# Optimization experiments

Hardware: AMD Instinct MI355X
Metric: run time of the kernel (lower is better)

The kernel has to match this reference:

```python
import jax, jax.numpy as jnp
import numpy as np
import math

B, S, N_UNITS, D_K = 8, 2048, 1024, 512


def setup_inputs() -> dict:
    key = jax.random.key(0)
    ks = jax.random.split(key, 8)
    scale = 1.0 / math.sqrt(N_UNITS)
    query = jax.random.normal(ks[0], (B, S, N_UNITS), dtype=jnp.float32)
    k_in = jax.random.normal(ks[1], (B, S, N_UNITS), dtype=jnp.float32)
    v_in = jax.random.normal(ks[2], (B, S, N_UNITS), dtype=jnp.float32)
    # custom multiplicative mask: causal lower-triangular, broadcast over batch
    mask = jnp.broadcast_to(jnp.tril(jnp.ones((S, S), dtype=jnp.float32)), (B, S, S))
    Wq = jax.random.normal(ks[3], (N_UNITS, D_K), dtype=jnp.float32) * scale
    Wk = jax.random.normal(ks[4], (N_UNITS, D_K), dtype=jnp.float32) * scale
    Wv = jax.random.normal(ks[5], (N_UNITS, D_K), dtype=jnp.float32) * scale
    bq = jnp.zeros((D_K,), dtype=jnp.float32)
    bk = jnp.zeros((D_K,), dtype=jnp.float32)
    bv = jnp.zeros((D_K,), dtype=jnp.float32)
    return {"query": query, "key": k_in, "value": v_in, "mask": mask,
            "Wq": Wq, "bq": bq, "Wk": Wk, "bk": bk, "Wv": Wv, "bv": bv}


def reference(query, key, value, mask, Wq, bq, Wk, bk, Wv, bv):
    d_k = Wq.shape[-1]
    Q = jnp.einsum('bsn,nd->bsd', query, Wq) + bq  # [B,S,Dk]
    K = jnp.einsum('bsn,nd->bsd', key, Wk) + bk
    V = jnp.einsum('bsn,nd->bsd', value, Wv) + bv
    # scores [B,S,S]
    x_hat = jnp.einsum('bqd,bkd->bqk', Q, K) / jnp.sqrt(jnp.float32(d_k))
    # custom multiplicative mask: x*mask - 1e9*(1-mask)
    x_hat_masked = x_hat * mask - 1e9 * (1.0 - mask)
    attn = jax.nn.softmax(x_hat_masked, axis=-1)
    # dropout = 0.0 (eval mode) -> identity
    out = jnp.einsum('bqk,bkd->bqd', attn, V)
    return out
```

## Files before the change

### kernel.cpp

```cpp
#include <hip/hip_runtime.h>

typedef __bf16 bf16_t;
typedef __attribute__((ext_vector_type(4))) __bf16 bf16x4;
typedef __attribute__((ext_vector_type(8))) __bf16 bf16x8;
typedef __attribute__((ext_vector_type(4))) float f32x4;

#define B_    8
#define S_    2048
#define NU    1024
#define DK    512
#define MROWS (B_ * S_)
#define PBATCH (128 * 128 * 136)

#define WAITVM(N) asm volatile("s_waitcnt vmcnt(" #N ")" ::: "memory")
#define WAITLG    asm volatile("s_waitcnt lgkmcnt(0)" ::: "memory")
#define BAR       asm volatile("s_barrier" ::: "memory")

__device__ __forceinline__ f32x4 mfma16(bf16x8 a, bf16x8 b, f32x4 c) {
  return __builtin_amdgcn_mfma_f32_16x16x32_bf16(a, b, c, 0, 0, 0);
}

__device__ __forceinline__ void async_load16(const void* g, void* l) {
  __builtin_amdgcn_global_load_lds(
      (const __attribute__((address_space(1))) unsigned int*)g,
      (__attribute__((address_space(3))) unsigned int*)l, 16, 0, 0);
}

__device__ __forceinline__ bf16x8 cvt8(f32x4 x0, f32x4 x1) {
  bf16x8 r;
#pragma unroll
  for (int j = 0; j < 4; ++j) { r[j] = (bf16_t)x0[j]; r[j + 4] = (bf16_t)x1[j]; }
  return r;
}

__device__ __forceinline__ void stage_tile(const bf16_t* __restrict__ src,
                                           int rstride, bf16_t* dst, int k0,
                                           int tid) {
#pragma unroll
  for (int j = 0; j < 2; ++j) {
    const int g = j * 256 + tid;
    const int ln = g >> 3, c = g & 7;
    const int cs = c ^ (ln & 7);
    const int srow = 2 * ln + (cs >> 2);
    async_load16(src + (size_t)srow * rstride + k0 + (cs & 3) * 8, dst + g * 8);
  }
}

__device__ __forceinline__ void stage_tile64(const bf16_t* __restrict__ src,
                                             int rstride, bf16_t* dst, int k0,
                                             int tid) {
  const int ln = tid >> 3, c = tid & 7;
  const int cs = c ^ (ln & 7);
  const int srow = 2 * ln + (cs >> 2);
  async_load16(src + (size_t)srow * rstride + k0 + (cs & 3) * 8, dst + tid * 8);
}

__device__ __forceinline__ bf16x8 frag(const bf16_t* buf, int row, int q) {
  const int ln = row >> 1;
  const int cp = (((row & 1) << 2) | q) ^ (ln & 7);
  return *(const bf16x8*)(buf + ln * 64 + cp * 8);
}

__global__ __launch_bounds__(256) void transpose_w_kernel(
    const float* __restrict__ Wq, const float* __restrict__ Wk,
    const float* __restrict__ Wv, bf16_t* __restrict__ Wt) {
  const float* W = (blockIdx.z == 0) ? Wq : (blockIdx.z == 1) ? Wk : Wv;
  bf16_t* Wo = Wt + (size_t)blockIdx.z * DK * NU;
  __shared__ float tile[32][33];
  const int t = threadIdx.x;
  const int r = t >> 5, c = t & 31;
  const int kbase = blockIdx.y * 32, nbase = blockIdx.x * 32;
#pragma unroll
  for (int i = 0; i < 4; ++i)
    tile[r + i * 8][c] = W[(size_t)(kbase + r + i * 8) * DK + nbase + c];
  __syncthreads();
#pragma unroll
  for (int i = 0; i < 4; ++i)
    Wo[(size_t)(nbase + r + i * 8) * NU + kbase + c] = (bf16_t)tile[c][r + i * 8];
}

__global__ __launch_bounds__(256, 2) void xw3_gemm_kernel(
    const float* __restrict__ q_in, const float* __restrict__ k_in,
    const float* __restrict__ v_in, const bf16_t* __restrict__ Wt,
    const float* __restrict__ bq, const float* __restrict__ bk,
    const float* __restrict__ bv, bf16_t* __restrict__ Qo,
    bf16_t* __restrict__ Ko, bf16_t* __restrict__ Vt) {
  const int bx = blockIdx.x;
  const int z = bx >> 9;
  const int t = bx & 511;
  const int m0 = (t & 127) * 128;
  const int n0 = (t >> 7) * 128;
  const float* X = (z == 0) ? q_in : (z == 1) ? k_in : v_in;
  const float* bias = (z == 0) ? bq : (z == 1) ? bk : bv;

  const int tid = threadIdx.x;
  const int wave = tid >> 6, lane = tid & 63;
  const int l16 = lane & 15, quad = lane >> 4;
  const int wm = (wave >> 1) * 64, wn = (wave & 1) * 64;

  __shared__ __align__(16) unsigned char smem[65536];
  bf16_t* ldsA = (bf16_t*)smem;
  bf16_t* ldsB = (bf16_t*)(smem + 32768);

  const float* Ag = X + (size_t)m0 * NU;
  const bf16_t* Bg = Wt + (size_t)z * DK * NU + (size_t)n0 * NU;

  int g0 = 2 * tid, g1 = 2 * tid + 1;
  const int cs0 = (g0 & 7) ^ ((g0 >> 3) & 7);
  const int cs1 = (g1 & 7) ^ ((g1 >> 3) & 7);
  const int sr0 = 2 * (g0 >> 3) + (cs0 >> 2), c40 = cs0 & 3;
  const int sr1 = 2 * (g1 >> 3) + (cs1 >> 2), c41 = cs1 & 3;
  const float* ap0 = Ag + (size_t)sr0 * NU + c40 * 8;
  const float* ap1 = Ag + (size_t)sr1 * NU + c41 * 8;

#define XW_A_LOAD(S, K0)                                                      \
  f32x4 xl##S##0 = *(const f32x4*)(ap0 + (K0));                               \
  f32x4 xl##S##1 = *(const f32x4*)(ap0 + (K0) + 4);                           \
  f32x4 xl##S##2 = *(const f32x4*)(ap1 + (K0));                               \
  f32x4 xl##S##3 = *(const f32x4*)(ap1 + (K0) + 4);
#define XW_A_WRITE(S, BUFE)                                                   \
  *(bf16x8*)&ldsA[(BUFE) + g0 * 8] = cvt8(xl##S##0, xl##S##1);                \
  *(bf16x8*)&ldsA[(BUFE) + g1 * 8] = cvt8(xl##S##2, xl##S##3);

  f32x4 acc[4][4] = {};

  {
    XW_A_LOAD(0, 0)
    XW_A_LOAD(1, 32)
    XW_A_LOAD(2, 64)
    XW_A_LOAD(3, 96)
    stage_tile(Bg, NU, ldsB, 0, tid);
    stage_tile(Bg, NU, ldsB + 4096, 32, tid);
    stage_tile(Bg, NU, ldsB + 8192, 64, tid);
    stage_tile(Bg, NU, ldsB + 12288, 96, tid);
    XW_A_WRITE(0, 0)
    XW_A_WRITE(1, 4096)
    XW_A_WRITE(2, 8192)
    XW_A_WRITE(3, 12288)
    WAITVM(0);
    WAITLG;
    BAR;
  }

  const int NS = 32;
  for (int j = 0; j < NS / 2; ++j) {
    const int ks2 = 2 * j;
    const int base = (j & 1) * 8192;
    bf16x8 af[2][4], bfr[2][4];
#pragma unroll
    for (int s = 0; s < 2; ++s)
#pragma unroll
      for (int i = 0; i < 4; ++i) {
        af[s][i] = frag(ldsA + base + s * 4096, wm + i * 16 + l16, quad);
        bfr[s][i] = frag(ldsB + base + s * 4096, wn + i * 16 + l16, quad);
      }
    WAITLG;
    BAR;
    const bool more = (ks2 + 4) < NS;
    if (more) {
      const int k4 = (ks2 + 4) * 32;
      XW_A_LOAD(4, k4)
      XW_A_LOAD(5, k4 + 32)
      stage_tile(Bg, NU, ldsB + base, k4, tid);
      stage_tile(Bg, NU, ldsB + base + 4096, k4 + 32, tid);
      __builtin_amdgcn_s_setprio(1);
#pragma unroll
      for (int s = 0; s < 2; ++s)
#pragma unroll
        for (int i = 0; i < 4; ++i)
#pragma unroll
          for (int jj = 0; jj < 4; ++jj)
            acc[i][jj] = mfma16(af[s][i], bfr[s][jj], acc[i][jj]);
      __builtin_amdgcn_s_setprio(0);
      WAITVM(4);
      XW_A_WRITE(4, base)
      XW_A_WRITE(5, base + 4096)
    } else {
      __builtin_amdgcn_s_setprio(1);
#pragma unroll
      for (int s = 0; s < 2; ++s)
#pragma unroll
        for (int i = 0; i < 4; ++i)
#pragma unroll
          for (int jj = 0; jj < 4; ++jj)
            acc[i][jj] = mfma16(af[s][i], bfr[s][jj], acc[i][jj]);
      __builtin_amdgcn_s_setprio(0);
      WAITVM(0);
    }
    WAITLG;
    BAR;
  }

  if (z != 2) {
    bf16_t* Out = (z == 0) ? Qo : Ko;
#pragma unroll
    for (int j = 0; j < 4; ++j) {
      const int cn = n0 + wn + j * 16 + l16;
      const float bz = bias[cn];
#pragma unroll
      for (int i = 0; i < 4; ++i) {
        const int rm = m0 + wm + i * 16 + quad * 4;
#pragma unroll
        for (int r = 0; r < 4; ++r)
          Out[(size_t)(rm + r) * DK + cn] = (bf16_t)(acc[i][j][r] + bz);
      }
    }
  } else {
    bf16_t* Ts = (bf16_t*)smem;
    BAR;
#pragma unroll
    for (int j = 0; j < 4; ++j) {
      const int cnl = wn + j * 16 + l16;
      const float bz = bias[n0 + cnl];
#pragma unroll
      for (int i = 0; i < 4; ++i) {
        const int rs = wm + i * 16 + quad * 4;
        bf16x4 tv;
#pragma unroll
        for (int r = 0; r < 4; ++r) tv[r] = (bf16_t)(acc[i][j][r] + bz);
        *(bf16x4*)&Ts[cnl * 136 + rs] = tv;
      }
    }
    WAITLG; BAR;
    const int bb2 = m0 >> 11, sl = m0 & 2047;
    const int row = tid >> 1, half = tid & 1;
    bf16_t* dst = Vt + ((size_t)bb2 * DK + n0 + row) * S_ + sl + half * 64;
    const bf16_t* sp = &Ts[row * 136 + half * 64];
#pragma unroll
    for (int k = 0; k < 8; ++k)
      *(bf16x8*)(dst + k * 8) = *(const bf16x8*)(sp + k * 8);
  }
#undef XW_A_LOAD
#undef XW_A_WRITE
}

__global__ __launch_bounds__(256, 2) void qk_p_kernel(
    const bf16_t* __restrict__ Q, const bf16_t* __restrict__ K,
    bf16_t* __restrict__ P, float* __restrict__ Lp) {
  const int bx = blockIdx.x;
  const int b = bx & 7;
  const int t = bx >> 3;
  int mt = 0;
  while (((mt + 1) * (mt + 2)) / 2 <= t) ++mt;
  const int nt = t - (mt * (mt + 1)) / 2;
  const int klen = (mt + 1) * 128;

  const int tid = threadIdx.x;
  const int wave = tid >> 6, lane = tid & 63;
  const int l16 = lane & 15, quad = lane >> 4;
  const int wm = (wave >> 1) * 64, wn = (wave & 1) * 64;

  __shared__ __align__(16) unsigned char smem[65536];
  bf16_t* ldsA = (bf16_t*)smem;
  bf16_t* ldsB = (bf16_t*)(smem + 32768);

  const bf16_t* Ag = Q + (size_t)(b * S_ + mt * 128) * DK;
  const bf16_t* Bg = K + (size_t)(b * S_ + nt * 128) * DK;

  f32x4 acc[4][4] = {};

  stage_tile(Ag, DK, ldsA, 0, tid);
  stage_tile(Bg, DK, ldsB, 0, tid);
  stage_tile(Ag, DK, ldsA + 4096, 32, tid);
  stage_tile(Bg, DK, ldsB + 4096, 32, tid);
  stage_tile(Ag, DK, ldsA + 8192, 64, tid);
  stage_tile(Bg, DK, ldsB + 8192, 64, tid);
  stage_tile(Ag, DK, ldsA + 12288, 96, tid);
  stage_tile(Bg, DK, ldsB + 12288, 96, tid);
  WAITVM(8);
  BAR;

  const int NS = 16;
  for (int j = 0; j < NS / 2; ++j) {
    const int ks2 = 2 * j;
    const int base = (j & 1) * 8192;
    bf16x8 af[2][4], bfr[2][4];
#pragma unroll
    for (int s = 0; s < 2; ++s)
#pragma unroll
      for (int i = 0; i < 4; ++i) {
        af[s][i] = frag(ldsA + base + s * 4096, wm + i * 16 + l16, quad);
        bfr[s][i] = frag(ldsB + base + s * 4096, wn + i * 16 + l16, quad);
      }
    WAITLG;
    BAR;
    const bool more = (ks2 + 4) < NS;
    if (more) {
      const int k4 = (ks2 + 4) * 32;
      stage_tile(Ag, DK, ldsA + base, k4, tid);
      stage_tile(Bg, DK, ldsB + base, k4, tid);
      stage_tile(Ag, DK, ldsA + base + 4096, k4 + 32, tid);
      stage_tile(Bg, DK, ldsB + base + 4096, k4 + 32, tid);
    }
    __builtin_amdgcn_s_setprio(1);
#pragma unroll
    for (int s = 0; s < 2; ++s)
#pragma unroll
      for (int i = 0; i < 4; ++i)
#pragma unroll
        for (int jj = 0; jj < 4; ++jj)
          acc[i][jj] = mfma16(af[s][i], bfr[s][jj], acc[i][jj]);
    __builtin_amdgcn_s_setprio(0);
    if (more) { WAITVM(8); } else { WAITVM(0); }
    BAR;
  }

  const float scale = 0.04419417382415922f;
  bf16_t* Pt = P + (size_t)b * PBATCH + (size_t)8192 * mt * (mt + 1);
  float* Lph = Lp + ((size_t)(b * 136 + t) * 2 + (wn >> 6)) * 128;
#pragma unroll
  for (int i = 0; i < 4; ++i) {
#pragma unroll
    for (int r = 0; r < 4; ++r) {
      const int lrow = wm + i * 16 + quad * 4 + r;
      const int srow = mt * 128 + lrow;
      float rsum = 0.f;
#pragma unroll
      for (int j = 0; j < 4; ++j) {
        const int scol = nt * 128 + wn + j * 16 + l16;
        const float p =
            (scol > srow) ? 0.f : __expf(acc[i][j][r] * scale - 10.0f);
        rsum += p;
        Pt[(size_t)lrow * klen + scol] = (bf16_t)p;
      }
#pragma unroll
      for (int off = 8; off >= 1; off >>= 1)
        rsum += __shfl_xor(rsum, off, 64);
      if (l16 == 0) Lph[lrow] = rsum;
    }
  }
}

__global__ __launch_bounds__(256, 3) void pv_kernel(
    const bf16_t* __restrict__ P, const bf16_t* __restrict__ Vt,
    const float* __restrict__ Lp, float* __restrict__ Out) {
  const int bx = blockIdx.x;
  const int low = bx & 63;
  const int b = low & 7;
  const int d0 = ((low >> 3) & 3) * 128;
  const int half = (low >> 5) & 1;
  const int g = bx >> 6;
  const int q2 = g >> 2, rb = g & 3;
  const int mt = (q2 == 0) ? 15 - 2 * rb
               : (q2 == 1) ? 2 * rb
               : (q2 == 2) ? 14 - 2 * rb
                           : 1 + 2 * rb;
  const int klen = (mt + 1) * 128;
  const int NS = (mt + 1) * 4;

  const int tid = threadIdx.x;
  const int wave = tid >> 6, lane = tid & 63;
  const int l16 = lane & 15, quad = lane >> 4;
  const int wm = (wave >> 1) * 32, wn = (wave & 1) * 64;

  __shared__ __align__(16) unsigned char smem[49664];
  bf16_t* ldsA = (bf16_t*)smem;
  bf16_t* ldsB = (bf16_t*)(smem + 16384);
  float* Ls = (float*)(smem + 49152);

  const bf16_t* Ag = P + (size_t)b * PBATCH + (size_t)8192 * mt * (mt + 1) +
                     (size_t)(half * 64) * klen;
  const bf16_t* Bg = Vt + ((size_t)b * DK + d0) * S_;

  f32x4 acc[2][4] = {};

  stage_tile64(Ag, klen, ldsA, 0, tid);
  stage_tile(Bg, S_, ldsB, 0, tid);
  stage_tile64(Ag, klen, ldsA + 2048, 32, tid);
  stage_tile(Bg, S_, ldsB + 4096, 32, tid);
  stage_tile64(Ag, klen, ldsA + 4096, 64, tid);
  stage_tile(Bg, S_, ldsB + 8192, 64, tid);
  stage_tile64(Ag, klen, ldsA + 6144, 96, tid);
  stage_tile(Bg, S_, ldsB + 12288, 96, tid);
  WAITVM(6);
  BAR;

  for (int j = 0; j < NS / 2; ++j) {
    const int ks2 = 2 * j;
    const int baseA = (j & 1) * 4096;
    const int baseB = (j & 1) * 8192;
    bf16x8 af[2][2], bfr[2][4];
#pragma unroll
    for (int s = 0; s < 2; ++s) {
#pragma unroll
      for (int i = 0; i < 2; ++i)
        af[s][i] = frag(ldsA + baseA + s * 2048, wm + i * 16 + l16, quad);
#pragma unroll
      for (int i = 0; i < 4; ++i)
        bfr[s][i] = frag(ldsB + baseB + s * 4096, wn + i * 16 + l16, quad);
    }
    WAITLG;
    BAR;
    const bool more = (ks2 + 4) < NS;
    if (more) {
      const int k4 = (ks2 + 4) * 32;
      stage_tile64(Ag, klen, ldsA + baseA, k4, tid);
      stage_tile(Bg, S_, ldsB + baseB, k4, tid);
      stage_tile64(Ag, klen, ldsA + baseA + 2048, k4 + 32, tid);
      stage_tile(Bg, S_, ldsB + baseB + 4096, k4 + 32, tid);
    }
    __builtin_amdgcn_s_setprio(1);
#pragma unroll
    for (int s = 0; s < 2; ++s)
#pragma unroll
      for (int i = 0; i < 2; ++i)
#pragma unroll
        for (int jj = 0; jj < 4; ++jj)
          acc[i][jj] = mfma16(af[s][i], bfr[s][jj], acc[i][jj]);
    __builtin_amdgcn_s_setprio(0);
    if (more) { WAITVM(6); } else { WAITVM(0); }
    BAR;
  }

  if (tid < 64) {
    const int rowit = half * 64 + tid;
    const float* lp =
        Lp + ((size_t)(b * 136 + (mt * (mt + 1)) / 2) * 2) * 128 + rowit;
    float s = 0.f;
    for (int n = 0; n <= mt; ++n) s += lp[n * 256] + lp[n * 256 + 128];
    Ls[tid] = s;
  }
  WAITLG; BAR;

  const int m0 = b * S_ + mt * 128 + half * 64;
#pragma unroll
  for (int i = 0; i < 2; ++i) {
#pragma unroll
    for (int r = 0; r < 4; ++r) {
      const int lr = wm + i * 16 + quad * 4 + r;
      const float inv = 1.0f / Ls[lr];
      float* orow = Out + (size_t)(m0 + lr) * DK + d0;
#pragma unroll
      for (int j = 0; j < 4; ++j)
        orow[wn + j * 16 + l16] = acc[i][j][r] * inv;
    }
  }
}

extern "C" void kernel_launch(void* const* d_in, const int* in_sizes, int n_in,
                              void* d_out, int out_size, void* d_ws, size_t ws_size,
                              hipStream_t stream) {
  const float* query = (const float*)d_in[0];
  const float* key_i = (const float*)d_in[1];
  const float* value = (const float*)d_in[2];
  const float* Wq = (const float*)d_in[4];
  const float* bq = (const float*)d_in[5];
  const float* Wk = (const float*)d_in[6];
  const float* bk = (const float*)d_in[7];
  const float* Wv = (const float*)d_in[8];
  const float* bv = (const float*)d_in[9];
  float* out = (float*)d_out;

  bf16_t* Wt = (bf16_t*)d_ws;
  bf16_t* Qw = Wt + (size_t)3 * DK * NU;
  bf16_t* Kw = Qw + (size_t)MROWS * DK;
  bf16_t* Vw = Kw + (size_t)MROWS * DK;
  bf16_t* Pw = Vw + (size_t)MROWS * DK;
  float* Lpw = (float*)(Pw + (size_t)B_ * PBATCH);

  transpose_w_kernel<<<dim3(16, 32, 3), 256, 0, stream>>>(Wq, Wk, Wv, Wt);
  xw3_gemm_kernel<<<1536, 256, 0, stream>>>(query, key_i, value, Wt, bq, bk,
                                            bv, Qw, Kw, Vw);
  qk_p_kernel<<<1088, 256, 0, stream>>>(Qw, Kw, Pw, Lpw);
  pv_kernel<<<1024, 256, 0, stream>>>(Pw, Vw, Lpw, out);
}
```

Measured before the change: 420.9 us.

## Permute key order to vectorize P stores; precompute row sums in separate kernel

```diff
diff --git a/kernel.cpp b/kernel.cpp
--- a/kernel.cpp
+++ b/kernel.cpp
@@ -53,6 +53,18 @@
   const int cs = c ^ (ln & 7);
   const int srow = 2 * ln + (cs >> 2);
   async_load16(src + (size_t)srow * rstride + k0 + (cs & 3) * 8, dst + tid * 8);
+}
+
+__device__ __forceinline__ void stage_tile_f32(const float* __restrict__ src,
+                                               int rstride, float* dst, int k0,
+                                               int tid) {
+#pragma unroll
+  for (int j = 0; j < 4; ++j) {
+    const int g = j * 256 + tid;
+    const int row = g >> 3, c = g & 7;
+    const int cs = c ^ (row & 7);
+    async_load16(src + (size_t)row * rstride + k0 + (cs << 2), dst + g * 4);
+  }
 }
 
 __device__ __forceinline__ bf16x8 frag(const bf16_t* buf, int row, int q) {
@@ -214,11 +226,11 @@
       const float bz = bias[n0 + cnl];
 #pragma unroll
       for (int i = 0; i < 4; ++i) {
-        const int rs = wm + i * 16 + quad * 4;
-        bf16x4 tv;
-#pragma unroll
-        for (int r = 0; r < 4; ++r) tv[r] = (bf16_t)(acc[i][j][r] + bz);
-        *(bf16x4*)&Ts[cnl * 136 + rs] = tv;
+#pragma unroll
+        for (int r = 0; r < 4; ++r) {
+          Ts[cnl * 136 + wm + quad * 16 + r * 4 + i] =
+              (bf16_t)(acc[i][j][r] + bz);
+        }
       }
     }
     WAITLG; BAR;
@@ -315,14 +327,16 @@
       const int lrow = wm + i * 16 + quad * 4 + r;
       const int srow = mt * 128 + lrow;
       float rsum = 0.f;
+      bf16x4 pk;
 #pragma unroll
       for (int j = 0; j < 4; ++j) {
         const int scol = nt * 128 + wn + j * 16 + l16;
         const float p =
             (scol > srow) ? 0.f : __expf(acc[i][j][r] * scale - 10.0f);
         rsum += p;
-        Pt[(size_t)lrow * klen + scol] = (bf16_t)p;
+        pk[j] = (bf16_t)p;
       }
+      *(bf16x4*)&Pt[(size_t)lrow * klen + nt * 128 + wn + l16 * 4] = pk;
 #pragma unroll
       for (int off = 8; off >= 1; off >>= 1)
         rsum += __shfl_xor(rsum, off, 64);
@@ -331,9 +345,23 @@
   }
 }
 
+__global__ __launch_bounds__(256) void lred_kernel(const float* __restrict__ Lp,
+                                                   float* __restrict__ L) {
+  const int row = blockIdx.x * 256 + threadIdx.x;
+  const int b = row >> 11;
+  const int wi = row & 2047;
+  const int mt = wi >> 7;
+  const int lrow = wi & 127;
+  const float* lp =
+      Lp + ((size_t)(b * 136 + (mt * (mt + 1)) / 2) * 2) * 128 + lrow;
+  float s = 0.f;
+  for (int n = 0; n <= mt; ++n) s += lp[n * 256] + lp[n * 256 + 128];
+  L[row] = s;
+}
+
 __global__ __launch_bounds__(256, 3) void pv_kernel(
     const bf16_t* __restrict__ P, const bf16_t* __restrict__ Vt,
-    const float* __restrict__ Lp, float* __restrict__ Out) {
+    const float* __restrict__ L, float* __restrict__ Out) {
   const int bx = blockIdx.x;
   const int low = bx & 63;
   const int b = low & 7;
@@ -353,10 +381,9 @@
   const int l16 = lane & 15, quad = lane >> 4;
   const int wm = (wave >> 1) * 32, wn = (wave & 1) * 64;
 
-  __shared__ __align__(16) unsigned char smem[49664];
+  __shared__ __align__(16) unsigned char smem[49152];
   bf16_t* ldsA = (bf16_t*)smem;
   bf16_t* ldsB = (bf16_t*)(smem + 16384);
-  float* Ls = (float*)(smem + 49152);
 
   const bf16_t* Ag = P + (size_t)b * PBATCH + (size_t)8192 * mt * (mt + 1) +
                      (size_t)(half * 64) * klen;
@@ -412,23 +439,13 @@
     BAR;
   }
 
-  if (tid < 64) {
-    const int rowit = half * 64 + tid;
-    const float* lp =
-        Lp + ((size_t)(b * 136 + (mt * (mt + 1)) / 2) * 2) * 128 + rowit;
-    float s = 0.f;
-    for (int n = 0; n <= mt; ++n) s += lp[n * 256] + lp[n * 256 + 128];
-    Ls[tid] = s;
-  }
-  WAITLG; BAR;
-
   const int m0 = b * S_ + mt * 128 + half * 64;
 #pragma unroll
   for (int i = 0; i < 2; ++i) {
 #pragma unroll
     for (int r = 0; r < 4; ++r) {
       const int lr = wm + i * 16 + quad * 4 + r;
-      const float inv = 1.0f / Ls[lr];
+      const float inv = 1.0f / L[m0 + lr];
       float* orow = Out + (size_t)(m0 + lr) * DK + d0;
 #pragma unroll
       for (int j = 0; j < 4; ++j)
@@ -457,10 +474,12 @@
   bf16_t* Vw = Kw + (size_t)MROWS * DK;
   bf16_t* Pw = Vw + (size_t)MROWS * DK;
   float* Lpw = (float*)(Pw + (size_t)B_ * PBATCH);
+  float* Lw = Lpw + (size_t)B_ * 136 * 2 * 128;
 
   transpose_w_kernel<<<dim3(16, 32, 3), 256, 0, stream>>>(Wq, Wk, Wv, Wt);
   xw3_gemm_kernel<<<1536, 256, 0, stream>>>(query, key_i, value, Wt, bq, bk,
                                             bv, Qw, Kw, Vw);
   qk_p_kernel<<<1088, 256, 0, stream>>>(Qw, Kw, Pw, Lpw);
-  pv_kernel<<<1024, 256, 0, stream>>>(Pw, Vw, Lpw, out);
-}
+  lred_kernel<<<64, 256, 0, stream>>>(Lpw, Lw);
+  pv_kernel<<<1024, 256, 0, stream>>>(Pw, Vw, Lw, out);
+}
```

New measurement: 426.5 us. Within noise of the previous version (+1.3%).

## Widen QK tiles to 128x256 with 512 threads and a triple-buffered pipeline

Applied to the files above, without the earlier changes.

```diff
diff --git a/kernel.cpp b/kernel.cpp
--- a/kernel.cpp
+++ b/kernel.cpp
@@ -53,6 +53,28 @@
   const int cs = c ^ (ln & 7);
   const int srow = 2 * ln + (cs >> 2);
   async_load16(src + (size_t)srow * rstride + k0 + (cs & 3) * 8, dst + tid * 8);
+}
+
+__device__ __forceinline__ void stage_a512(const bf16_t* __restrict__ src,
+                                           int rstride, bf16_t* dst, int k0,
+                                           int tid) {
+  const int ln = tid >> 3, c = tid & 7;
+  const int cs = c ^ (ln & 7);
+  const int srow = 2 * ln + (cs >> 2);
+  async_load16(src + (size_t)srow * rstride + k0 + (cs & 3) * 8, dst + tid * 8);
+}
+
+__device__ __forceinline__ void stage_b512(const bf16_t* __restrict__ src,
+                                           int rstride, bf16_t* dst, int k0,
+                                           int tid) {
+#pragma unroll
+  for (int j = 0; j < 2; ++j) {
+    const int g = j * 512 + tid;
+    const int ln = g >> 3, c = g & 7;
+    const int cs = c ^ (ln & 7);
+    const int srow = 2 * ln + (cs >> 2);
+    async_load16(src + (size_t)srow * rstride + k0 + (cs & 3) * 8, dst + g * 8);
+  }
 }
 
 __device__ __forceinline__ bf16x8 frag(const bf16_t* buf, int row, int q) {
@@ -234,80 +256,72 @@
 #undef XW_A_WRITE
 }
 
-__global__ __launch_bounds__(256, 2) void qk_p_kernel(
+__global__ __launch_bounds__(512, 4) void qk_p_kernel(
     const bf16_t* __restrict__ Q, const bf16_t* __restrict__ K,
     bf16_t* __restrict__ P, float* __restrict__ Lp) {
   const int bx = blockIdx.x;
   const int b = bx & 7;
   const int t = bx >> 3;
-  int mt = 0;
-  while (((mt + 1) * (mt + 2)) / 2 <= t) ++mt;
-  const int nt = t - (mt * (mt + 1)) / 2;
+  int mt = 0, base0 = 0, np = 1;
+  while (base0 + np <= t) { base0 += np; ++mt; np = (mt + 2) / 2; }
+  const int nt0 = 2 * (t - base0);
   const int klen = (mt + 1) * 128;
 
   const int tid = threadIdx.x;
   const int wave = tid >> 6, lane = tid & 63;
   const int l16 = lane & 15, quad = lane >> 4;
-  const int wm = (wave >> 1) * 64, wn = (wave & 1) * 64;
-
-  __shared__ __align__(16) unsigned char smem[65536];
+  const int wm = (wave >> 2) * 64;
+  const int wn2 = (wave & 3) * 64;
+
+  __shared__ __align__(16) unsigned char smem[73728];
   bf16_t* ldsA = (bf16_t*)smem;
-  bf16_t* ldsB = (bf16_t*)(smem + 32768);
+  bf16_t* ldsB = (bf16_t*)(smem + 24576);
 
   const bf16_t* Ag = Q + (size_t)(b * S_ + mt * 128) * DK;
-  const bf16_t* Bg = K + (size_t)(b * S_ + nt * 128) * DK;
+  const bf16_t* Bg = K + (size_t)(b * S_ + nt0 * 128) * DK;
 
   f32x4 acc[4][4] = {};
 
-  stage_tile(Ag, DK, ldsA, 0, tid);
-  stage_tile(Bg, DK, ldsB, 0, tid);
-  stage_tile(Ag, DK, ldsA + 4096, 32, tid);
-  stage_tile(Bg, DK, ldsB + 4096, 32, tid);
-  stage_tile(Ag, DK, ldsA + 8192, 64, tid);
-  stage_tile(Bg, DK, ldsB + 8192, 64, tid);
-  stage_tile(Ag, DK, ldsA + 12288, 96, tid);
-  stage_tile(Bg, DK, ldsB + 12288, 96, tid);
-  WAITVM(8);
+  stage_a512(Ag, DK, ldsA, 0, tid);
+  stage_b512(Bg, DK, ldsB, 0, tid);
+  stage_a512(Ag, DK, ldsA + 4096, 32, tid);
+  stage_b512(Bg, DK, ldsB + 8192, 32, tid);
+  stage_a512(Ag, DK, ldsA + 8192, 64, tid);
+  stage_b512(Bg, DK, ldsB + 16384, 64, tid);
+  WAITVM(6);
   BAR;
 
   const int NS = 16;
-  for (int j = 0; j < NS / 2; ++j) {
-    const int ks2 = 2 * j;
-    const int base = (j & 1) * 8192;
-    bf16x8 af[2][4], bfr[2][4];
-#pragma unroll
-    for (int s = 0; s < 2; ++s)
-#pragma unroll
-      for (int i = 0; i < 4; ++i) {
-        af[s][i] = frag(ldsA + base + s * 4096, wm + i * 16 + l16, quad);
-        bfr[s][i] = frag(ldsB + base + s * 4096, wn + i * 16 + l16, quad);
-      }
+  for (int j = 0; j < NS; ++j) {
+    const int m3 = j % 3;
+    bf16x8 af[4], bfr[4];
+#pragma unroll
+    for (int i = 0; i < 4; ++i) {
+      af[i] = frag(ldsA + m3 * 4096, wm + i * 16 + l16, quad);
+      bfr[i] = frag(ldsB + m3 * 8192, wn2 + i * 16 + l16, quad);
+    }
     WAITLG;
     BAR;
-    const bool more = (ks2 + 4) < NS;
-    if (more) {
-      const int k4 = (ks2 + 4) * 32;
-      stage_tile(Ag, DK, ldsA + base, k4, tid);
-      stage_tile(Bg, DK, ldsB + base, k4, tid);
-      stage_tile(Ag, DK, ldsA + base + 4096, k4 + 32, tid);
-      stage_tile(Bg, DK, ldsB + base + 4096, k4 + 32, tid);
+    if (j + 3 < NS) {
+      stage_a512(Ag, DK, ldsA + m3 * 4096, (j + 3) * 32, tid);
+      stage_b512(Bg, DK, ldsB + m3 * 8192, (j + 3) * 32, tid);
     }
     __builtin_amdgcn_s_setprio(1);
 #pragma unroll
-    for (int s = 0; s < 2; ++s)
-#pragma unroll
-      for (int i = 0; i < 4; ++i)
-#pragma unroll
-        for (int jj = 0; jj < 4; ++jj)
-          acc[i][jj] = mfma16(af[s][i], bfr[s][jj], acc[i][jj]);
+    for (int i = 0; i < 4; ++i)
+#pragma unroll
+      for (int jj = 0; jj < 4; ++jj)
+        acc[i][jj] = mfma16(af[i], bfr[jj], acc[i][jj]);
     __builtin_amdgcn_s_setprio(0);
-    if (more) { WAITVM(8); } else { WAITVM(0); }
+    if (j + 3 < NS) { WAITVM(6); }
+    else if (j + 2 < NS) { WAITVM(3); }
+    else { WAITVM(0); }
     BAR;
   }
 
   const float scale = 0.04419417382415922f;
   bf16_t* Pt = P + (size_t)b * PBATCH + (size_t)8192 * mt * (mt + 1);
-  float* Lph = Lp + ((size_t)(b * 136 + t) * 2 + (wn >> 6)) * 128;
+  float* Lph = Lp + ((size_t)(b * 72 + t) * 4 + (wave & 3)) * 128;
 #pragma unroll
   for (int i = 0; i < 4; ++i) {
 #pragma unroll
@@ -317,11 +331,11 @@
       float rsum = 0.f;
 #pragma unroll
       for (int j = 0; j < 4; ++j) {
-        const int scol = nt * 128 + wn + j * 16 + l16;
+        const int scol = nt0 * 128 + wn2 + j * 16 + l16;
         const float p =
             (scol > srow) ? 0.f : __expf(acc[i][j][r] * scale - 10.0f);
         rsum += p;
-        Pt[(size_t)lrow * klen + scol] = (bf16_t)p;
+        if (scol < klen) Pt[(size_t)lrow * klen + scol] = (bf16_t)p;
       }
 #pragma unroll
       for (int off = 8; off >= 1; off >>= 1)
@@ -414,10 +428,14 @@
 
   if (tid < 64) {
     const int rowit = half * 64 + tid;
-    const float* lp =
-        Lp + ((size_t)(b * 136 + (mt * (mt + 1)) / 2) * 2) * 128 + rowit;
+    const int k2 = mt >> 1;
+    const int cmt = (mt & 1) ? (k2 + 1) * (k2 + 1) : k2 * (k2 + 1);
+    const int cnt = (mt + 2) / 2;
+    const float* lp = Lp + ((size_t)(b * 72 + cmt) * 4) * 128 + rowit;
     float s = 0.f;
-    for (int n = 0; n <= mt; ++n) s += lp[n * 256] + lp[n * 256 + 128];
+    for (int p = 0; p < cnt; ++p)
+#pragma unroll
+      for (int h = 0; h < 4; ++h) s += lp[(p * 4 + h) * 128];
     Ls[tid] = s;
   }
   WAITLG; BAR;
@@ -461,6 +479,6 @@
   transpose_w_kernel<<<dim3(16, 32, 3), 256, 0, stream>>>(Wq, Wk, Wv, Wt);
   xw3_gemm_kernel<<<1536, 256, 0, stream>>>(query, key_i, value, Wt, bq, bk,
                                             bv, Qw, Kw, Vw);
-  qk_p_kernel<<<1088, 256, 0, stream>>>(Qw, Kw, Pw, Lpw);
+  qk_p_kernel<<<576, 512, 0, stream>>>(Qw, Kw, Pw, Lpw);
   pv_kernel<<<1024, 256, 0, stream>>>(Pw, Vw, Lpw, out);
 }
```

Result: no change. 421.9 us (+0.2%).
